# Kernel optimization log

Hardware: AMD Instinct MI355X
Metric: run time of the kernel (lower is better)

Reference implementation:

```python
import jax, jax.numpy as jnp
import numpy as np

N, T, D = 32, 64, 16
F = 512  # object_classes == feature dim after object_fc


def _gcn(x, adj, W, b):
    # Kipf GraphConvolution: adj @ (x @ W) + b
    return adj @ (x @ W) + b


def _norm_adj(a):
    d = jnp.sum(a, axis=1) ** -0.5
    return a * d[:, None] * d[None, :]


def _per_graph(x, gc1_W, gc1_b, gc2_W, gc2_b, gc3_W, gc3_b, gc4_W, gc4_b):
    # x: [D, F]
    # graph_generator / adj2: softmax-style similarity adjacency with D^{-1/2} norm
    s = x @ x.T                                   # [D, D]
    a = jnp.exp(s - jnp.max(s, axis=1, keepdims=True))
    adj = _norm_adj(a)
    # branch 1
    x1 = jax.nn.relu(_gcn(x, adj, gc1_W, gc1_b))
    x1 = _gcn(x1, adj, gc2_W, gc2_b)
    # branch 2 (adj_hat2 identical construction from x)
    y2 = jax.nn.relu(_gcn(x, adj, gc3_W, gc3_b))  # [D, 32]
    y22 = y2 @ y2.T
    nrm = jnp.sqrt(jnp.sum(y22 * y22, axis=1, keepdims=True))  # torch.norm(y22, 2, dim=1)
    adj3 = 1.0 + y22 / (nrm @ nrm.T)
    adj_hat3 = _norm_adj(adj3)
    y2 = _gcn(y2, adj_hat3, gc4_W, gc4_b)
    return (x1 + y2) * 0.5


def setup_inputs() -> dict:
    key = jax.random.key(0)
    ks = jax.random.split(key, 12)
    s = 0.02
    return {
        "object_raw": jax.random.normal(ks[0], (N * T * D, F), jnp.float32),
        "action_raw": jax.random.normal(ks[1], (N * T, F), jnp.float32),
        "W_obj": jax.random.normal(ks[2], (F, 512), jnp.float32) * s,
        "b_obj": jnp.zeros((512,), jnp.float32),
        "W_act": jax.random.normal(ks[3], (F, 512), jnp.float32) * s,
        "b_act": jnp.zeros((512,), jnp.float32),
        "gc1_W": jax.random.normal(ks[4], (512, 32), jnp.float32) * s,
        "gc1_b": jnp.zeros((32,), jnp.float32),
        "gc2_W": jax.random.normal(ks[5], (32, 512), jnp.float32) * s,
        "gc2_b": jnp.zeros((512,), jnp.float32),
        "gc3_W": jax.random.normal(ks[6], (512, 32), jnp.float32) * s,
        "gc3_b": jnp.zeros((32,), jnp.float32),
        "gc4_W": jax.random.normal(ks[7], (32, 512), jnp.float32) * s,
        "gc4_b": jnp.zeros((512,), jnp.float32),
        "fc1_W": jax.random.normal(ks[8], (512, 1024), jnp.float32) * s,
        "fc1_b": jnp.zeros((1024,), jnp.float32),
        "clf_W": jax.random.normal(ks[9], (1024, 500), jnp.float32) * s,
        "clf_b": jnp.zeros((500,), jnp.float32),
    }


def reference(object_raw, action_raw, W_obj, b_obj, W_act, b_act,
              gc1_W, gc1_b, gc2_W, gc2_b, gc3_W, gc3_b, gc4_W, gc4_b,
              fc1_W, fc1_b, clf_W, clf_b):
    obj = jax.nn.relu(object_raw @ W_obj + b_obj).reshape(N * T, D, 512)
    act = jax.nn.relu(action_raw @ W_act + b_act)           # [N*T, 512]
    obj = obj.at[:, D // 2].set(act)                         # overwrite middle frame
    graph = jax.vmap(lambda x: _per_graph(x, gc1_W, gc1_b, gc2_W, gc2_b,
                                          gc3_W, gc3_b, gc4_W, gc4_b))(obj)
    g = graph.reshape(N, T, D, 512).mean(axis=2)
    o = obj.reshape(N, T, D, 512).mean(axis=2)
    feat = (o + g) * 0.5                                     # graph_fusion == 'mean'
    c = jax.nn.relu(feat)                                    # dropout = identity (eval)
    c = jax.nn.relu(c @ fc1_W + fc1_b)
    out = (c @ clf_W + clf_b).mean(axis=1)                   # mean over T -> [N, 500]
    return out
```

## Files before the change

### kernel.cpp

```cpp
#include <hip/hip_runtime.h>
#include <hip/hip_bf16.h>

using ushort_t = unsigned short;
using f32x4  = __attribute__((ext_vector_type(4))) float;
using short8 = __attribute__((ext_vector_type(8))) short;

__device__ __forceinline__ float bflo(unsigned p) {
    union { unsigned u; float f; } x; x.u = p << 16; return x.f;
}
__device__ __forceinline__ float bfhi(unsigned p) {
    union { unsigned u; float f; } x; x.u = p & 0xffff0000u; return x.f;
}
__device__ __forceinline__ ushort_t f2bf(float f) {
    __hip_bfloat16 h = __float2bfloat16(f);
    return *(ushort_t*)&h;
}
__device__ __forceinline__ unsigned pk2bf(float lo, float hi) {
    __hip_bfloat162 h = __float22bfloat162_rn({lo, hi});
    return *(unsigned*)&h;
}

__device__ __forceinline__ void tr_tile(const float* __restrict__ S, ushort_t* __restrict__ D,
                                        int K, int N, int Npad, int bx, int by,
                                        int tx, int ty, float* tile )
{
    const int k0 = by * 32, n0 = bx * 32;
#pragma unroll
    for (int r = 0; r < 4; r++) {
        const int k = k0 + ty + r * 8, n = n0 + tx;
        tile[(ty + r * 8) * 33 + tx] = (k < K && n < N) ? S[(size_t)k * N + n] : 0.f;
    }
    __syncthreads();
#pragma unroll
    for (int r = 0; r < 4; r++) {
        const int n = n0 + ty + r * 8, k = k0 + tx;
        if (n < Npad && k < K) D[(size_t)n * K + k] = f2bf(tile[tx * 33 + ty + r * 8]);
    }
}

__global__ __launch_bounds__(256)
void prep_weights(const float* __restrict__ Wobj, ushort_t* __restrict__ WobjT,
                  const float* __restrict__ Wact, ushort_t* __restrict__ WactT,
                  const float* __restrict__ fc1W, ushort_t* __restrict__ fc1T,
                  const float* __restrict__ gc1W, ushort_t* __restrict__ W1t,
                  const float* __restrict__ gc3W, ushort_t* __restrict__ W3t,
                  const float* __restrict__ gc2W, ushort_t* __restrict__ W2bf,
                  const float* __restrict__ gc4W, ushort_t* __restrict__ W4bf)
{
    __shared__ float tile[32 * 33];
    const int b = blockIdx.x;
    const int t = threadIdx.x;
    const int tx = t & 31, ty = t >> 5;

    if (b < 1056) {
        const float* S; ushort_t* D; int K, N, Npad, nt, l;
        if      (b < 256)  { S = Wobj; D = WobjT; K = 512; N = 512;  Npad = 512;  nt = 16; l = b; }
        else if (b < 512)  { S = Wact; D = WactT; K = 512; N = 512;  Npad = 512;  nt = 16; l = b - 256; }
        else if (b < 1024) { S = fc1W; D = fc1T;  K = 512; N = 1024; Npad = 1024; nt = 32; l = b - 512; }
        else if (b < 1040) { S = gc1W; D = W1t;   K = 512; N = 32;   Npad = 32;   nt = 1;  l = b - 1024; }
        else               { S = gc3W; D = W3t;   K = 512; N = 32;   Npad = 32;   nt = 1;  l = b - 1040; }
        tr_tile(S, D, K, N, Npad, l % nt, l / nt, tx, ty, tile);
    } else {
        const float* S = (b < 1064) ? gc2W : gc4W;
        ushort_t* D    = (b < 1064) ? W2bf : W4bf;
        const int i = (b < 1064 ? b - 1056 : b - 1064) * 256 + t;
        const float4 x = ((const float4*)S)[2 * i];
        const float4 y = ((const float4*)S)[2 * i + 1];
        unsigned r[4] = { pk2bf(x.x, x.y), pk2bf(x.z, x.w), pk2bf(y.x, y.y), pk2bf(y.z, y.w) };
        ((uint4*)D)[i] = *(uint4*)r;
    }
}

__global__ __launch_bounds__(512, 2)
void gemm_obj_stream(const float* __restrict__ A, const ushort_t* __restrict__ Bt,
                     const float* __restrict__ bias, ushort_t* __restrict__ C)
{
    __shared__ __align__(16) ushort_t As[128 * 512];
    const int t = threadIdx.x;
    const int lane = t & 63, w = t >> 6;
    const int bm = blockIdx.x * 128;
    const int fr = lane & 15, fq = lane >> 4;

    const float4* A4 = (const float4*)(A + (size_t)bm * 512);
#pragma unroll
    for (int i = 0; i < 16; i++) {
        const int fl = i * 1024 + t * 2;
        const int row = fl >> 7;
        const float4 p0 = A4[fl];
        const float4 p1 = A4[fl + 1];
        unsigned rr[4] = { pk2bf(p0.x, p0.y), pk2bf(p0.z, p0.w),
                           pk2bf(p1.x, p1.y), pk2bf(p1.z, p1.w) };
        *(uint4*)&As[row * 512 + ((lane ^ (row & 7)) * 8)] = *(uint4*)rr;
    }

    const int nw = w * 64;
    const ushort_t* Bbase = Bt + (size_t)(nw + fr) * 512 + fq * 8;

    uint4 bA[4], bB[4];
#pragma unroll
    for (int j = 0; j < 4; j++) bA[j] = *(const uint4*)(Bbase + (size_t)j * 16 * 512);

    __syncthreads();

    f32x4 acc[4][8];
#pragma unroll
    for (int j = 0; j < 4; j++)
#pragma unroll
        for (int i = 0; i < 8; i++) acc[j][i] = (f32x4){0.f, 0.f, 0.f, 0.f};

    for (int kk = 0; kk < 16; kk += 2) {
        short8 af[8];
#pragma unroll
        for (int i = 0; i < 8; i++)
            af[i] = *(const short8*)&As[(i * 16 + fr) * 512 + (((kk * 4 + fq) ^ (fr & 7)) * 8)];
#pragma unroll
        for (int j = 0; j < 4; j++) {
            bB[j] = *(const uint4*)(Bbase + (size_t)j * 16 * 512 + (kk + 1) * 32);
            const short8 bf = *(const short8*)&bA[j];
#pragma unroll
            for (int i = 0; i < 8; i++)
                acc[j][i] = __builtin_amdgcn_mfma_f32_16x16x32_bf16(af[i], bf, acc[j][i], 0, 0, 0);
        }
#pragma unroll
        for (int i = 0; i < 8; i++)
            af[i] = *(const short8*)&As[(i * 16 + fr) * 512 + ((((kk + 1) * 4 + fq) ^ (fr & 7)) * 8)];
#pragma unroll
        for (int j = 0; j < 4; j++) {
            if (kk + 2 < 16)
                bA[j] = *(const uint4*)(Bbase + (size_t)j * 16 * 512 + (kk + 2) * 32);
            const short8 bf = *(const short8*)&bB[j];
#pragma unroll
            for (int i = 0; i < 8; i++)
                acc[j][i] = __builtin_amdgcn_mfma_f32_16x16x32_bf16(af[i], bf, acc[j][i], 0, 0, 0);
        }
    }

    __syncthreads();
#pragma unroll
    for (int j = 0; j < 4; j++) {
        const int col0 = j * 16 + fr;
        const float bv = bias[nw + col0];
#pragma unroll
        for (int i = 0; i < 8; i++) {
#pragma unroll
            for (int rr2 = 0; rr2 < 4; rr2++) {
                const int m = i * 16 + fq * 4 + rr2;
                const int pc = col0 ^ (((m >> 2) & 3) << 4);
                As[m * 512 + nw + pc] = f2bf(fmaxf(acc[j][i][rr2] + bv, 0.f));
            }
        }
    }
    __syncthreads();
#pragma unroll
    for (int i2 = 0; i2 < 16; i2++) {
        const int fl = i2 * 512 + t;
        const int m  = fl >> 6;
        const int n0 = (fl & 63) * 8;
        const int sl = n0 & ~63;
        const int cl = n0 & 63;
        const uint4 v = *(const uint4*)&As[m * 512 + sl + (cl ^ (((m >> 2) & 3) << 4))];
        *(uint4*)&C[(size_t)(bm + m) * 512 + n0] = v;
    }
}

typedef __attribute__((address_space(1))) void glb_void;
typedef __attribute__((address_space(3))) void lds_void;
__device__ __forceinline__ void dma16(const void* g, void* l) {
    __builtin_amdgcn_global_load_lds((glb_void*)(unsigned long long)(uintptr_t)g,
                                     (lds_void*)(unsigned)(uintptr_t)l, 16, 0, 0);
}

template<int RELU, typename AT>
__global__ __launch_bounds__(256)
void gemm_dma(const AT* __restrict__ A, const ushort_t* __restrict__ Bt,
              const float* __restrict__ bias, ushort_t* __restrict__ C,
              int N, int K, int Nb, int row_mul, int row_add)
{
    __shared__ __align__(16) char     AsRaw[128 * 32 * sizeof(AT)];
    __shared__ __align__(16) ushort_t Bs[128 * 32];
    const int t = threadIdx.x;
    const int lane = t & 63, w = t >> 6;
    const int bm = blockIdx.y * 128, bn = blockIdx.x * 128;
    const int mb = (w & 1) * 64, nb = (w >> 1) * 64;
    const int fr = lane & 15, fq = lane >> 4;

    f32x4 acc[16];
#pragma unroll
    for (int i = 0; i < 16; i++) acc[i] = (f32x4){0.f, 0.f, 0.f, 0.f};

    const int brow = lane >> 2, bk = lane & 3;
    const int klog = bk ^ ((brow >> 1) & 3);
    const int arow = lane >> 3, ag = lane & 7;

    for (int k0 = 0; k0 < K; k0 += 32) {
        __syncthreads();
        if constexpr (sizeof(AT) == 4) {
#pragma unroll
            for (int i = 0; i < 4; i++) {
                const int grp = w * 4 + i;
                const int row = grp * 8 + arow;
                const int gl = ag ^ (row & 7);
                dma16((const float*)A + (size_t)(bm + row) * K + k0 + gl * 4,
                      AsRaw + grp * 1024);
            }
        } else {
#pragma unroll
            for (int i = 0; i < 2; i++) {
                const int grp = w * 2 + i;
                const int row = grp * 16 + brow;
                dma16((const ushort_t*)A + (size_t)(bm + row) * K + k0 + klog * 8,
                      (ushort_t*)AsRaw + grp * 512);
            }
        }
#pragma unroll
        for (int i = 0; i < 2; i++) {
            const int grp = w * 2 + i;
            const int row = grp * 16 + brow;
            dma16(Bt + (size_t)(bn + row) * K + k0 + klog * 8, Bs + grp * 512);
        }
        __syncthreads();

        short8 af[4], bf[4];
        if constexpr (sizeof(AT) == 4) {
#pragma unroll
            for (int i = 0; i < 4; i++) {
                const int row = mb + i * 16 + fr;
                const float* base = (const float*)AsRaw + row * 32;
                const f32x4 p0 = *(const f32x4*)(base + (((2 * fq)     ^ (fr & 7)) * 4));
                const f32x4 p1 = *(const f32x4*)(base + (((2 * fq + 1) ^ (fr & 7)) * 4));
                unsigned rr[4] = { pk2bf(p0.x, p0.y), pk2bf(p0.z, p0.w),
                                   pk2bf(p1.x, p1.y), pk2bf(p1.z, p1.w) };
                af[i] = *(short8*)rr;
            }
        } else {
#pragma unroll
            for (int i = 0; i < 4; i++) {
                const int row = mb + i * 16 + fr;
                af[i] = *(const short8*)((const ushort_t*)AsRaw + row * 32 + (fq ^ ((fr >> 1) & 3)) * 8);
            }
        }
#pragma unroll
        for (int j = 0; j < 4; j++) {
            const int row = nb + j * 16 + fr;
            bf[j] = *(const short8*)(Bs + row * 32 + (fq ^ ((fr >> 1) & 3)) * 8);
        }
#pragma unroll
        for (int i = 0; i < 4; i++)
#pragma unroll
            for (int j = 0; j < 4; j++)
                acc[i * 4 + j] = __builtin_amdgcn_mfma_f32_16x16x32_bf16(
                    af[i], bf[j], acc[i * 4 + j], 0, 0, 0);
    }

#pragma unroll
    for (int j = 0; j < 4; j++) {
        const int n = bn + nb + j * 16 + fr;
        const float bv = (n < Nb) ? bias[n] : 0.f;
#pragma unroll
        for (int i = 0; i < 4; i++) {
            const f32x4 a = acc[i * 4 + j];
#pragma unroll
            for (int r = 0; r < 4; r++) {
                const int m = bm + mb + i * 16 + fq * 4 + r;
                float v = a[r] + bv;
                if (RELU) v = fmaxf(v, 0.f);
                C[((size_t)m * row_mul + row_add) * (size_t)N + n] = f2bf(v);
            }
        }
    }
}

__global__ __launch_bounds__(64)
void graph_mfma(const ushort_t* __restrict__ obj,
                const ushort_t* __restrict__ W1t, const float* __restrict__ b1,
                const ushort_t* __restrict__ W2b, const float* __restrict__ b2,
                const ushort_t* __restrict__ W3t, const float* __restrict__ b3,
                const ushort_t* __restrict__ W4b, const float* __restrict__ b4,
                ushort_t* __restrict__ cbuf)
{
    __shared__ float ssb[16 * 17];
    __shared__ float adjt[16 * 20];
    __shared__ float t1s[16 * 36];
    __shared__ float t3s[16 * 36];
    __shared__ float x1s[16 * 36];
    __shared__ float y2s[16 * 36];
    __shared__ float y22s[16 * 17];
    __shared__ float a3t[16 * 20];
    __shared__ float dv[16], dv3[16], nrm[16], cA[16], cA3[16];
    __shared__ float zc1[32], zc4[32];

    const int lane = threadIdx.x;
    const int r = lane & 15, fq = lane >> 4;
    const ushort_t* xg = obj + (size_t)blockIdx.x * 8192;

    short8 xf[16];
#pragma unroll
    for (int kk = 0; kk < 16; kk++)
        xf[kk] = *(const short8*)(xg + r * 512 + kk * 32 + fq * 8);

    f32x4 sacc = (f32x4){0.f, 0.f, 0.f, 0.f};
#pragma unroll
    for (int kk = 0; kk < 16; kk++)
        sacc = __builtin_amdgcn_mfma_f32_16x16x32_bf16(xf[kk], xf[kk], sacc, 0, 0, 0);

    f32x4 a10 = (f32x4){0.f,0.f,0.f,0.f}, a11 = a10, a30 = a10, a31 = a10;
#pragma unroll
    for (int kk = 0; kk < 16; kk++) {
        const short8 w10 = *(const short8*)(W1t + (size_t)(r)      * 512 + kk * 32 + fq * 8);
        const short8 w11 = *(const short8*)(W1t + (size_t)(16 + r) * 512 + kk * 32 + fq * 8);
        const short8 w30 = *(const short8*)(W3t + (size_t)(r)      * 512 + kk * 32 + fq * 8);
        const short8 w31 = *(const short8*)(W3t + (size_t)(16 + r) * 512 + kk * 32 + fq * 8);
        a10 = __builtin_amdgcn_mfma_f32_16x16x32_bf16(xf[kk], w10, a10, 0, 0, 0);
        a11 = __builtin_amdgcn_mfma_f32_16x16x32_bf16(xf[kk], w11, a11, 0, 0, 0);
        a30 = __builtin_amdgcn_mfma_f32_16x16x32_bf16(xf[kk], w30, a30, 0, 0, 0);
        a31 = __builtin_amdgcn_mfma_f32_16x16x32_bf16(xf[kk], w31, a31, 0, 0, 0);
    }

#pragma unroll
    for (int i = 0; i < 4; i++) {
        const int m = fq * 4 + i;
        ssb[m * 17 + r] = sacc[i];
        t1s[m * 36 + r]      = a10[i];
        t1s[m * 36 + 16 + r] = a11[i];
        t3s[m * 36 + r]      = a30[i];
        t3s[m * 36 + 16 + r] = a31[i];
    }
    __syncthreads();

    if (lane < 16) {
        float m = ssb[lane * 17];
#pragma unroll
        for (int j = 1; j < 16; j++) m = fmaxf(m, ssb[lane * 17 + j]);
        float s = 0.f;
#pragma unroll
        for (int j = 0; j < 16; j++) {
            const float e = expf(ssb[lane * 17 + j] - m);
            ssb[lane * 17 + j] = e; s += e;
        }
        dv[lane] = rsqrtf(s);
    }
    __syncthreads();

    {
        const float di = dv[r];
#pragma unroll
        for (int p = 0; p < 4; p++) {
            const int j = fq * 4 + p;
            adjt[j * 20 + r] = ssb[r * 17 + j] * di * dv[j];
        }
    }
    __syncthreads();

    if (lane < 16) {
        float s = 0.f;
#pragma unroll
        for (int i = 0; i < 16; i++) s += adjt[lane * 20 + i];
        cA[lane] = s;
    }

    {
        const int c = lane & 31, hi = lane >> 5;
        const float bb1 = b1[c], bb3 = b3[c];
        float ax[8], ay[8];
#pragma unroll
        for (int i = 0; i < 8; i++) { ax[i] = bb1; ay[i] = bb3; }
#pragma unroll
        for (int j = 0; j < 16; j++) {
            const float t1v = t1s[j * 36 + c], t3v = t3s[j * 36 + c];
            const float4 p = *(const float4*)&adjt[j * 20 + hi * 8];
            const float4 q = *(const float4*)&adjt[j * 20 + hi * 8 + 4];
            ax[0] = fmaf(p.x, t1v, ax[0]); ax[1] = fmaf(p.y, t1v, ax[1]);
            ax[2] = fmaf(p.z, t1v, ax[2]); ax[3] = fmaf(p.w, t1v, ax[3]);
            ax[4] = fmaf(q.x, t1v, ax[4]); ax[5] = fmaf(q.y, t1v, ax[5]);
            ax[6] = fmaf(q.z, t1v, ax[6]); ax[7] = fmaf(q.w, t1v, ax[7]);
            ay[0] = fmaf(p.x, t3v, ay[0]); ay[1] = fmaf(p.y, t3v, ay[1]);
            ay[2] = fmaf(p.z, t3v, ay[2]); ay[3] = fmaf(p.w, t3v, ay[3]);
            ay[4] = fmaf(q.x, t3v, ay[4]); ay[5] = fmaf(q.y, t3v, ay[5]);
            ay[6] = fmaf(q.z, t3v, ay[6]); ay[7] = fmaf(q.w, t3v, ay[7]);
        }
#pragma unroll
        for (int i = 0; i < 8; i++) {
            x1s[(hi * 8 + i) * 36 + c] = fmaxf(ax[i], 0.f);
            y2s[(hi * 8 + i) * 36 + c] = fmaxf(ay[i], 0.f);
        }
    }
    __syncthreads();

    {
        const int i2 = lane >> 2, j0 = (lane & 3) * 4;
        float a4[4] = {0.f, 0.f, 0.f, 0.f};
#pragma unroll
        for (int k4 = 0; k4 < 8; k4++) {
            const float4 yi = *(const float4*)&y2s[i2 * 36 + k4 * 4];
#pragma unroll
            for (int p = 0; p < 4; p++) {
                const float4 yj = *(const float4*)&y2s[(j0 + p) * 36 + k4 * 4];
                a4[p] = fmaf(yi.x, yj.x, a4[p]); a4[p] = fmaf(yi.y, yj.y, a4[p]);
                a4[p] = fmaf(yi.z, yj.z, a4[p]); a4[p] = fmaf(yi.w, yj.w, a4[p]);
            }
        }
#pragma unroll
        for (int p = 0; p < 4; p++) y22s[i2 * 17 + j0 + p] = a4[p];
    }
    __syncthreads();

    if (lane < 16) {
        float sq = 0.f;
#pragma unroll
        for (int j = 0; j < 16; j++) { const float v = y22s[lane * 17 + j]; sq = fmaf(v, v, sq); }
        nrm[lane] = sqrtf(sq);
    }
    __syncthreads();

    {
        const float ni = nrm[r];
#pragma unroll
        for (int p = 0; p < 4; p++) {
            const int j = fq * 4 + p;
            a3t[j * 20 + r] = 1.0f + y22s[r * 17 + j] / (ni * nrm[j]);
        }
    }
    __syncthreads();

    if (lane < 16) {
        float s = 0.f;
#pragma unroll
        for (int j = 0; j < 16; j++) s += a3t[j * 20 + lane];
        dv3[lane] = rsqrtf(s);
    }
    __syncthreads();

    if (lane < 16) {
        float s = 0.f;
#pragma unroll
        for (int i = 0; i < 16; i++) s = fmaf(a3t[lane * 20 + i], dv3[i], s);
        cA3[lane] = s * dv3[lane];
    }
    __syncthreads();

    if (lane < 32) {
        float s1 = 0.f, s4 = 0.f;
#pragma unroll
        for (int j = 0; j < 16; j++) {
            s1 = fmaf(cA[j],  x1s[j * 36 + lane], s1);
            s4 = fmaf(cA3[j], y2s[j * 36 + lane], s4);
        }
        zc1[lane] = s1; zc4[lane] = s4;
    }
    __syncthreads();

    {
        float om[8] = {0,0,0,0,0,0,0,0};
#pragma unroll
        for (int m = 0; m < 16; m++) {
            const uint4 q = *(const uint4*)(xg + m * 512 + lane * 8);
            om[0] += bflo(q.x); om[1] += bfhi(q.x);
            om[2] += bflo(q.y); om[3] += bfhi(q.y);
            om[4] += bflo(q.z); om[5] += bfhi(q.z);
            om[6] += bflo(q.w); om[7] += bfhi(q.w);
        }
        float gm[8] = {0,0,0,0,0,0,0,0};
        for (int k = 0; k < 32; k++) {
            const float z1 = zc1[k], z4 = zc4[k];
            const uint4 w2 = *(const uint4*)(W2b + (size_t)k * 512 + lane * 8);
            const uint4 w4 = *(const uint4*)(W4b + (size_t)k * 512 + lane * 8);
            gm[0] = fmaf(z1, bflo(w2.x), gm[0]); gm[0] = fmaf(z4, bflo(w4.x), gm[0]);
            gm[1] = fmaf(z1, bfhi(w2.x), gm[1]); gm[1] = fmaf(z4, bfhi(w4.x), gm[1]);
            gm[2] = fmaf(z1, bflo(w2.y), gm[2]); gm[2] = fmaf(z4, bflo(w4.y), gm[2]);
            gm[3] = fmaf(z1, bfhi(w2.y), gm[3]); gm[3] = fmaf(z4, bfhi(w4.y), gm[3]);
            gm[4] = fmaf(z1, bflo(w2.z), gm[4]); gm[4] = fmaf(z4, bflo(w4.z), gm[4]);
            gm[5] = fmaf(z1, bfhi(w2.z), gm[5]); gm[5] = fmaf(z4, bfhi(w4.z), gm[5]);
            gm[6] = fmaf(z1, bflo(w2.w), gm[6]); gm[6] = fmaf(z4, bflo(w4.w), gm[6]);
            gm[7] = fmaf(z1, bfhi(w2.w), gm[7]); gm[7] = fmaf(z4, bfhi(w4.w), gm[7]);
        }
        const float4 b2a = *(const float4*)&b2[lane * 8];
        const float4 b2b = *(const float4*)&b2[lane * 8 + 4];
        const float4 b4a = *(const float4*)&b4[lane * 8];
        const float4 b4b = *(const float4*)&b4[lane * 8 + 4];
        const float bs[8] = { b2a.x + b4a.x, b2a.y + b4a.y, b2a.z + b4a.z, b2a.w + b4a.w,
                              b2b.x + b4b.x, b2b.y + b4b.y, b2b.z + b4b.z, b2b.w + b4b.w };
        ushort_t pk[8];
#pragma unroll
        for (int c = 0; c < 8; c++) {
            const float gmean = 0.5f * bs[c] + gm[c] * (1.0f / 32.0f);
            const float feat  = 0.5f * (om[c] * 0.0625f + gmean);
            pk[c] = f2bf(fmaxf(feat, 0.f));
        }
        *(uint4*)(cbuf + (size_t)blockIdx.x * 512 + lane * 8) = *(uint4*)pk;
    }
}

__global__ __launch_bounds__(256)
void mean_c2(const ushort_t* __restrict__ c2, float* __restrict__ cmean)
{
    const int idx = blockIdx.x * 256 + threadIdx.x;
    const int n = idx >> 10, k = idx & 1023;
    const ushort_t* p = c2 + (size_t)n * 64 * 1024 + k;
    float s = 0.f;
#pragma unroll 8
    for (int tt = 0; tt < 64; tt++) {
        union { unsigned u; float f; } x; x.u = ((unsigned)p[tt * 1024]) << 16;
        s += x.f;
    }
    cmean[idx] = s * (1.0f / 64.0f);
}

__global__ __launch_bounds__(256)
void clf_col(const float* __restrict__ cmean, const float* __restrict__ W,
             const float* __restrict__ clf_b, float* __restrict__ out)
{
    __shared__ float red[8][33];
    const int j = blockIdx.x;
    const int t = threadIdx.x;
    const int n = t & 31, kp = t >> 5;
    const float* cm = cmean + (size_t)n * 1024 + kp * 128;
    const float* wp = W + (size_t)kp * 128 * 500 + j;
    float acc = 0.f;
#pragma unroll
    for (int k = 0; k < 128; k += 4) {
        const float4 c = *(const float4*)(cm + k);
        acc = fmaf(c.x, wp[(size_t)(k + 0) * 500], acc);
        acc = fmaf(c.y, wp[(size_t)(k + 1) * 500], acc);
        acc = fmaf(c.z, wp[(size_t)(k + 2) * 500], acc);
        acc = fmaf(c.w, wp[(size_t)(k + 3) * 500], acc);
    }
    red[kp][n] = acc;
    __syncthreads();
    if (t < 32) {
        float s = red[0][t];
#pragma unroll
        for (int p = 1; p < 8; p++) s += red[p][t];
        out[(size_t)t * 500 + j] = s + clf_b[j];
    }
}

extern "C" void kernel_launch(void* const* d_in, const int* in_sizes, int n_in,
                              void* d_out, int out_size, void* d_ws, size_t ws_size,
                              hipStream_t stream)
{
    const float* object_raw = (const float*)d_in[0];
    const float* action_raw = (const float*)d_in[1];
    const float* W_obj = (const float*)d_in[2];
    const float* b_obj = (const float*)d_in[3];
    const float* W_act = (const float*)d_in[4];
    const float* b_act = (const float*)d_in[5];
    const float* gc1_W = (const float*)d_in[6];
    const float* gc1_b = (const float*)d_in[7];
    const float* gc2_W = (const float*)d_in[8];
    const float* gc2_b = (const float*)d_in[9];
    const float* gc3_W = (const float*)d_in[10];
    const float* gc3_b = (const float*)d_in[11];
    const float* gc4_W = (const float*)d_in[12];
    const float* gc4_b = (const float*)d_in[13];
    const float* fc1_W = (const float*)d_in[14];
    const float* fc1_b = (const float*)d_in[15];
    const float* clf_W = (const float*)d_in[16];
    const float* clf_b = (const float*)d_in[17];

    char* ws = (char*)d_ws;
    const size_t MB = 1024 * 1024;
    ushort_t* obj_bf = (ushort_t*)(ws);
    ushort_t* cbuf   = (ushort_t*)(ws + 32 * MB);
    ushort_t* c2     = (ushort_t*)(ws + 34 * MB);
    float*    cmean  = (float*)   (ws + 38 * MB);
    ushort_t* WobjT  = (ushort_t*)(ws + 39 * MB);
    ushort_t* WactT  = (ushort_t*)(ws + 39 * MB + 512 * 1024);
    ushort_t* fc1T   = (ushort_t*)(ws + 40 * MB);
    ushort_t* W1t    = (ushort_t*)(ws + 41 * MB);
    ushort_t* W3t    = (ushort_t*)(ws + 41 * MB + 32 * 1024);
    ushort_t* W2bf   = (ushort_t*)(ws + 41 * MB + 64 * 1024);
    ushort_t* W4bf   = (ushort_t*)(ws + 41 * MB + 96 * 1024);

    prep_weights<<<dim3(1072), 256, 0, stream>>>(
        W_obj, WobjT, W_act, WactT, fc1_W, fc1T,
        gc1_W, W1t, gc3_W, W3t, gc2_W, W2bf, gc4_W, W4bf);

    gemm_obj_stream<<<dim3(256), 512, 0, stream>>>(object_raw, WobjT, b_obj, obj_bf);

    gemm_dma<1, float><<<dim3(4, 16), 256, 0, stream>>>(
        action_raw, WactT, b_act, obj_bf, 512, 512, 512, 16, 8);

    graph_mfma<<<dim3(2048), 64, 0, stream>>>(
        obj_bf, W1t, gc1_b, W2bf, gc2_b, W3t, gc3_b, W4bf, gc4_b, cbuf);

    gemm_dma<1, ushort_t><<<dim3(8, 16), 256, 0, stream>>>(
        cbuf, fc1T, fc1_b, c2, 1024, 512, 1024, 1, 0);

    mean_c2<<<dim3(128), 256, 0, stream>>>(c2, cmean);

    clf_col<<<dim3(500), 256, 0, stream>>>(cmean, clf_W, clf_b, (float*)d_out);
}
```

Measured before the change: 241.8 us.

## Fuse fc1 GEMM with mean over T and pre-transpose classifier weights

Adds a dedicated fc1 GEMM kernel whose epilogue applies bias and ReLU, then reduces the 64 rows of each batch item in registers and with shuffles to write the per-sample mean directly. This removes the bf16 c2 intermediate buffer and the separate mean kernel launch. It also transposes clf_W into a float workspace inside prep_weights so clf_col can read weights with contiguous float4 loads instead of strided scalar loads. The cost is 512 extra transpose blocks in prep_weights on every call.

```diff
diff --git a/kernel.cpp b/kernel.cpp
--- a/kernel.cpp
+++ b/kernel.cpp
@@ -35,6 +35,24 @@
     for (int r = 0; r < 4; r++) {
         const int n = n0 + ty + r * 8, k = k0 + tx;
         if (n < Npad && k < K) D[(size_t)n * K + k] = f2bf(tile[tx * 33 + ty + r * 8]);
+    }
+}
+
+__device__ __forceinline__ void trf_tile(const float* __restrict__ S, float* __restrict__ D,
+                                         int K, int N, int bx, int by,
+                                         int tx, int ty, float* tile )
+{
+    const int k0 = by * 32, n0 = bx * 32;
+#pragma unroll
+    for (int r = 0; r < 4; r++) {
+        const int k = k0 + ty + r * 8, n = n0 + tx;
+        tile[(ty + r * 8) * 33 + tx] = (k < K && n < N) ? S[(size_t)k * N + n] : 0.f;
+    }
+    __syncthreads();
+#pragma unroll
+    for (int r = 0; r < 4; r++) {
+        const int n = n0 + ty + r * 8, k = k0 + tx;
+        if (n < N && k < K) D[(size_t)n * K + k] = tile[tx * 33 + ty + r * 8];
     }
 }
 
@@ -45,7 +63,8 @@
                   const float* __restrict__ gc1W, ushort_t* __restrict__ W1t,
                   const float* __restrict__ gc3W, ushort_t* __restrict__ W3t,
                   const float* __restrict__ gc2W, ushort_t* __restrict__ W2bf,
-                  const float* __restrict__ gc4W, ushort_t* __restrict__ W4bf)
+                  const float* __restrict__ gc4W, ushort_t* __restrict__ W4bf,
+                  const float* __restrict__ clfW, float* __restrict__ WclfT)
 {
     __shared__ float tile[32 * 33];
     const int b = blockIdx.x;
@@ -60,7 +79,7 @@
         else if (b < 1040) { S = gc1W; D = W1t;   K = 512; N = 32;   Npad = 32;   nt = 1;  l = b - 1024; }
         else               { S = gc3W; D = W3t;   K = 512; N = 32;   Npad = 32;   nt = 1;  l = b - 1040; }
         tr_tile(S, D, K, N, Npad, l % nt, l / nt, tx, ty, tile);
-    } else {
+    } else if (b < 1072) {
         const float* S = (b < 1064) ? gc2W : gc4W;
         ushort_t* D    = (b < 1064) ? W2bf : W4bf;
         const int i = (b < 1064 ? b - 1056 : b - 1064) * 256 + t;
@@ -68,6 +87,9 @@
         const float4 y = ((const float4*)S)[2 * i + 1];
         unsigned r[4] = { pk2bf(x.x, x.y), pk2bf(x.z, x.w), pk2bf(y.x, y.y), pk2bf(y.z, y.w) };
         ((uint4*)D)[i] = *(uint4*)r;
+    } else {
+        const int l = b - 1072;
+        trf_tile(clfW, WclfT, 1024, 500, l & 15, l >> 4, tx, ty, tile);
     }
 }
 
@@ -267,6 +289,79 @@
                 C[((size_t)m * row_mul + row_add) * (size_t)N + n] = f2bf(v);
             }
         }
+    }
+}
+
+__global__ __launch_bounds__(256)
+void gemm_fc1_mean(const ushort_t* __restrict__ A, const ushort_t* __restrict__ Bt,
+                   const float* __restrict__ bias, float* __restrict__ cmean)
+{
+    __shared__ __align__(16) ushort_t AsS[128 * 32];
+    __shared__ __align__(16) ushort_t Bs[128 * 32];
+    const int t = threadIdx.x;
+    const int lane = t & 63, w = t >> 6;
+    const int bm = blockIdx.y * 128, bn = blockIdx.x * 128;
+    const int mb = (w & 1) * 64, nb = (w >> 1) * 64;
+    const int fr = lane & 15, fq = lane >> 4;
+    const int K = 512;
+
+    f32x4 acc[16];
+#pragma unroll
+    for (int i = 0; i < 16; i++) acc[i] = (f32x4){0.f, 0.f, 0.f, 0.f};
+
+    const int brow = lane >> 2, bk = lane & 3;
+    const int klog = bk ^ ((brow >> 1) & 3);
+
+    for (int k0 = 0; k0 < K; k0 += 32) {
+        __syncthreads();
+#pragma unroll
+        for (int i = 0; i < 2; i++) {
+            const int grp = w * 2 + i;
+            const int row = grp * 16 + brow;
+            dma16(A + (size_t)(bm + row) * K + k0 + klog * 8, AsS + grp * 512);
+        }
+#pragma unroll
+        for (int i = 0; i < 2; i++) {
+            const int grp = w * 2 + i;
+            const int row = grp * 16 + brow;
+            dma16(Bt + (size_t)(bn + row) * K + k0 + klog * 8, Bs + grp * 512);
+        }
+        __syncthreads();
+
+        short8 af[4], bf[4];
+#pragma unroll
+        for (int i = 0; i < 4; i++) {
+            const int row = mb + i * 16 + fr;
+            af[i] = *(const short8*)(AsS + row * 32 + (fq ^ ((fr >> 1) & 3)) * 8);
+        }
+#pragma unroll
+        for (int j = 0; j < 4; j++) {
+            const int row = nb + j * 16 + fr;
+            bf[j] = *(const short8*)(Bs + row * 32 + (fq ^ ((fr >> 1) & 3)) * 8);
+        }
+#pragma unroll
+        for (int i = 0; i < 4; i++)
+#pragma unroll
+            for (int j = 0; j < 4; j++)
+                acc[i * 4 + j] = __builtin_amdgcn_mfma_f32_16x16x32_bf16(
+                    af[i], bf[j], acc[i * 4 + j], 0, 0, 0);
+    }
+
+    const int nidx = (bm + mb) >> 6;
+#pragma unroll
+    for (int j = 0; j < 4; j++) {
+        const int n = bn + nb + j * 16 + fr;
+        const float bv = bias[n];
+        float s = 0.f;
+#pragma unroll
+        for (int i = 0; i < 4; i++) {
+            const f32x4 a = acc[i * 4 + j];
+#pragma unroll
+            for (int r = 0; r < 4; r++) s += fmaxf(a[r] + bv, 0.f);
+        }
+        s += __shfl_xor(s, 16);
+        s += __shfl_xor(s, 32);
+        if (fq == 0) cmean[(size_t)nidx * 1024 + n] = s * (1.0f / 64.0f);
     }
 }
 
@@ -491,22 +586,7 @@
 }
 
 __global__ __launch_bounds__(256)
-void mean_c2(const ushort_t* __restrict__ c2, float* __restrict__ cmean)
-{
-    const int idx = blockIdx.x * 256 + threadIdx.x;
-    const int n = idx >> 10, k = idx & 1023;
-    const ushort_t* p = c2 + (size_t)n * 64 * 1024 + k;
-    float s = 0.f;
-#pragma unroll 8
-    for (int tt = 0; tt < 64; tt++) {
-        union { unsigned u; float f; } x; x.u = ((unsigned)p[tt * 1024]) << 16;
-        s += x.f;
-    }
-    cmean[idx] = s * (1.0f / 64.0f);
-}
-
-__global__ __launch_bounds__(256)
-void clf_col(const float* __restrict__ cmean, const float* __restrict__ W,
+void clf_col(const float* __restrict__ cmean, const float* __restrict__ Wt,
              const float* __restrict__ clf_b, float* __restrict__ out)
 {
     __shared__ float red[8][33];
@@ -514,15 +594,16 @@
     const int t = threadIdx.x;
     const int n = t & 31, kp = t >> 5;
     const float* cm = cmean + (size_t)n * 1024 + kp * 128;
-    const float* wp = W + (size_t)kp * 128 * 500 + j;
+    const float* wp = Wt + (size_t)j * 1024 + kp * 128;
     float acc = 0.f;
 #pragma unroll
     for (int k = 0; k < 128; k += 4) {
         const float4 c = *(const float4*)(cm + k);
-        acc = fmaf(c.x, wp[(size_t)(k + 0) * 500], acc);
-        acc = fmaf(c.y, wp[(size_t)(k + 1) * 500], acc);
-        acc = fmaf(c.z, wp[(size_t)(k + 2) * 500], acc);
-        acc = fmaf(c.w, wp[(size_t)(k + 3) * 500], acc);
+        const float4 wv = *(const float4*)(wp + k);
+        acc = fmaf(c.x, wv.x, acc);
+        acc = fmaf(c.y, wv.y, acc);
+        acc = fmaf(c.z, wv.z, acc);
+        acc = fmaf(c.w, wv.w, acc);
     }
     red[kp][n] = acc;
     __syncthreads();
@@ -561,7 +642,7 @@
     const size_t MB = 1024 * 1024;
     ushort_t* obj_bf = (ushort_t*)(ws);
     ushort_t* cbuf   = (ushort_t*)(ws + 32 * MB);
-    ushort_t* c2     = (ushort_t*)(ws + 34 * MB);
+    float*    WclfT  = (float*)   (ws + 34 * MB);
     float*    cmean  = (float*)   (ws + 38 * MB);
     ushort_t* WobjT  = (ushort_t*)(ws + 39 * MB);
     ushort_t* WactT  = (ushort_t*)(ws + 39 * MB + 512 * 1024);
@@ -571,9 +652,10 @@
     ushort_t* W2bf   = (ushort_t*)(ws + 41 * MB + 64 * 1024);
     ushort_t* W4bf   = (ushort_t*)(ws + 41 * MB + 96 * 1024);
 
-    prep_weights<<<dim3(1072), 256, 0, stream>>>(
+    prep_weights<<<dim3(1584), 256, 0, stream>>>(
         W_obj, WobjT, W_act, WactT, fc1_W, fc1T,
-        gc1_W, W1t, gc3_W, W3t, gc2_W, W2bf, gc4_W, W4bf);
+        gc1_W, W1t, gc3_W, W3t, gc2_W, W2bf, gc4_W, W4bf,
+        clf_W, WclfT);
 
     gemm_obj_stream<<<dim3(256), 512, 0, stream>>>(object_raw, WobjT, b_obj, obj_bf);
 
@@ -583,10 +665,7 @@
     graph_mfma<<<dim3(2048), 64, 0, stream>>>(
         obj_bf, W1t, gc1_b, W2bf, gc2_b, W3t, gc3_b, W4bf, gc4_b, cbuf);
 
-    gemm_dma<1, ushort_t><<<dim3(8, 16), 256, 0, stream>>>(
-        cbuf, fc1T, fc1_b, c2, 1024, 512, 1024, 1, 0);
-
-    mean_c2<<<dim3(128), 256, 0, stream>>>(c2, cmean);
-
-    clf_col<<<dim3(500), 256, 0, stream>>>(cmean, clf_W, clf_b, (float*)d_out);
-}
+    gemm_fc1_mean<<<dim3(8, 16), 256, 0, stream>>>(cbuf, fc1T, fc1_b, cmean);
+
+    clf_col<<<dim3(500), 256, 0, stream>>>(cmean, WclfT, clf_b, (float*)d_out);
+}
```

Measured after the change: 229.0 us. 1.06x faster.
